# Performance work log

Hardware: AMD Instinct MI355X
Metric: run time of the kernel (lower is better)

The kernel has to match this reference:

```python
import jax, jax.numpy as jnp
import numpy as np

B, DIM, K, NH = 65536, 8, 64, 100
TOTAL = DIM * K


def setup_inputs() -> dict:
    key = jax.random.key(0)
    ks = jax.random.split(key, 14)
    e = jax.random.normal(ks[0], (B, DIM, K), dtype=jnp.float32)
    # strictly upper-triangular DAG adjacency: C[j, i] = 1 iff j < i (j is a parent of i)
    C = jnp.triu(jnp.ones((DIM, DIM), dtype=jnp.int32), k=1)
    sc = 0.05
    inp = {"e": e, "C": C}
    inp["sW1"] = jax.random.normal(ks[1], (TOTAL, NH), dtype=jnp.float32) * sc
    inp["sb1"] = jnp.zeros((NH,), dtype=jnp.float32)
    inp["sW2"] = jax.random.normal(ks[2], (NH, NH), dtype=jnp.float32) * sc
    inp["sb2"] = jnp.zeros((NH,), dtype=jnp.float32)
    inp["sW3"] = jax.random.normal(ks[3], (NH, K), dtype=jnp.float32) * sc
    inp["sb3"] = jnp.zeros((K,), dtype=jnp.float32)
    inp["tW1"] = jax.random.normal(ks[4], (TOTAL, NH), dtype=jnp.float32) * sc
    inp["tb1"] = jnp.zeros((NH,), dtype=jnp.float32)
    inp["tW2"] = jax.random.normal(ks[5], (NH, NH), dtype=jnp.float32) * sc
    inp["tb2"] = jnp.zeros((NH,), dtype=jnp.float32)
    inp["tW3"] = jax.random.normal(ks[6], (NH, K), dtype=jnp.float32) * sc
    inp["tb3"] = jnp.zeros((K,), dtype=jnp.float32)
    return inp


def _mlp(x, mask, W1, b1, W2, b2, W3, b3):
    # MLP.forward: net(x * mask); Linear->ReLU->Linear->ReLU->Linear->Sigmoid
    h = jax.nn.relu((x * mask) @ W1 + b1)
    h = jax.nn.relu(h @ W2 + b2)
    return jax.nn.sigmoid(h @ W3 + b3)


def reference(e, C, sW1, sb1, sW2, sb2, sW3, sb3, tW1, tb1, tW2, tb2, tW3, tb3):
    b, dim, k = e.shape
    total = dim * k
    # mask for step i: column C[:, i] with each entry repeated k times -> [total]
    # (if column i is all zeros, mask is zeros, matching the elif branch)
    masks = jnp.repeat(C.astype(e.dtype), k, axis=0).T  # [dim, total]
    e_steps = jnp.swapaxes(e, 0, 1)  # [dim, B, k]

    def step(z, xs):
        i, mask, e_i = xs
        zf = z.reshape(b, total)
        s = _mlp(zf, mask, sW1, sb1, sW2, sb2, sW3, sb3)  # [B, k]
        t = _mlp(zf, mask, tW1, tb1, tW2, tb2, tW3, tb3)  # [B, k]
        z = z.at[:, i, :].set(jnp.exp(s) * e_i + t)
        return z, jnp.sum(s, axis=1)

    z0 = jnp.zeros_like(e)
    z, ld_steps = jax.lax.scan(step, z0, (jnp.arange(dim), masks, e_steps))
    log_det = jnp.sum(ld_steps, axis=0)  # [B]
    return z, log_det
```

## Files before the change

### kernel.cpp

```cpp
#include <hip/hip_runtime.h>

#define B_SZ 65536
#define NH   100

typedef __bf16 bf16_t;
typedef __bf16 bf16x2 __attribute__((ext_vector_type(2)));
typedef __bf16 bf16x8 __attribute__((ext_vector_type(8)));
typedef float  f32x4  __attribute__((ext_vector_type(4)));

#define SZ_W2 14336
#define SZ_W3 8192
#define SZ_W1 7168
#define OFF_W3   28672
#define OFF_W1   45056
#define WS_TOTAL 145408

__global__ void prep_weights(const float* __restrict__ sW1, const float* __restrict__ sW2,
                             const float* __restrict__ sW3, const float* __restrict__ tW1,
                             const float* __restrict__ tW2, const float* __restrict__ tW3,
                             bf16_t* __restrict__ ws) {
  int idx = blockIdx.x * 256 + threadIdx.x;
  if (idx >= WS_TOTAL) return;
  float v = 0.f;
  if (idx < 2 * SZ_W2) {
    const float* W = (idx < SZ_W2) ? sW2 : tW2;
    int l = (idx < SZ_W2) ? idx : idx - SZ_W2;
    int j = l & 7, ln = (l >> 3) & 63, kc = (l >> 9) & 3, mt = l >> 11;
    int k = kc * 32 + (ln >> 4) * 8 + j;
    int m = mt * 16 + (ln & 15);
    v = (k < NH && m < NH) ? W[k * NH + m] : 0.f;
  } else if (idx < OFF_W1) {
    int l = idx - OFF_W3;
    const float* W = (l < SZ_W3) ? sW3 : tW3;
    l &= (SZ_W3 - 1);
    int j = l & 7, ln = (l >> 3) & 63, kc = (l >> 9) & 3, mt = l >> 11;
    int k = kc * 32 + (ln >> 4) * 8 + j;
    int m = mt * 16 + (ln & 15);
    v = (k < NH) ? W[k * 64 + m] : 0.f;
  } else {
    int l = idx - OFF_W1;
    int b = l / (2 * SZ_W1);
    int r2 = l - b * 2 * SZ_W1;
    const float* W = (r2 < SZ_W1) ? sW1 : tW1;
    int w = (r2 < SZ_W1) ? r2 : r2 - SZ_W1;
    int j = w & 7, ln = (w >> 3) & 63, kc = (w >> 9) & 1, mt = w >> 10;
    int k = kc * 32 + (ln >> 4) * 8 + j;
    int m = mt * 16 + (ln & 15);
    v = (m < NH) ? W[(b * 64 + k) * NH + m] : 0.f;
  }
  ws[idx] = (bf16_t)v;
}

__global__ void prep_bias(const float* __restrict__ sb1, const float* __restrict__ sb2,
                          const float* __restrict__ sb3, const float* __restrict__ tb1,
                          const float* __restrict__ tb2, const float* __restrict__ tb3,
                          float* __restrict__ fb) {
  int t = threadIdx.x;
  if (t < 112)       fb[t] = (t < NH) ? sb2[t] : 0.f;
  else if (t < 224)  fb[t] = (t - 112 < NH) ? tb2[t - 112] : 0.f;
  else if (t < 288)  fb[t] = sb3[t - 224];
  else if (t < 352)  fb[t] = tb3[t - 288];
  else if (t < 464)  fb[t] = (t - 352 < NH) ? sb1[t - 352] : 0.f;
  else if (t < 576)  fb[t] = (t - 464 < NH) ? tb1[t - 464] : 0.f;
}

__device__ __forceinline__ void gload_lds16(const void* gptr, void* lptr) {
  __builtin_amdgcn_global_load_lds(
      (const __attribute__((address_space(1))) unsigned int*)gptr,
      (__attribute__((address_space(3))) unsigned int*)lptr, 16, 0, 0);
}

__device__ __forceinline__ unsigned pk2(float a, float b) {
  bf16x2 t = {(bf16_t)a, (bf16_t)b};
  return __builtin_bit_cast(unsigned, t);
}

__device__ __forceinline__ bf16x8 build_bfrag(const unsigned* pkLo, const unsigned* pkHi,
                                              int idx0, int idx1, bool hiSel) {
  int l0 = __builtin_amdgcn_ds_bpermute(idx0, (int)pkLo[0]);
  int h0 = __builtin_amdgcn_ds_bpermute(idx0, (int)pkHi[0]);
  int l1 = __builtin_amdgcn_ds_bpermute(idx0, (int)pkLo[1]);
  int h1 = __builtin_amdgcn_ds_bpermute(idx0, (int)pkHi[1]);
  int l2 = __builtin_amdgcn_ds_bpermute(idx1, (int)pkLo[0]);
  int h2 = __builtin_amdgcn_ds_bpermute(idx1, (int)pkHi[0]);
  int l3 = __builtin_amdgcn_ds_bpermute(idx1, (int)pkLo[1]);
  int h3 = __builtin_amdgcn_ds_bpermute(idx1, (int)pkHi[1]);
  union { unsigned u[4]; bf16x8 v; } r;
  r.u[0] = (unsigned)(hiSel ? h0 : l0);
  r.u[1] = (unsigned)(hiSel ? h1 : l1);
  r.u[2] = (unsigned)(hiSel ? h2 : l2);
  r.u[3] = (unsigned)(hiSel ? h3 : l3);
  return r.v;
}

struct __align__(16) SMem {
  bf16_t w2[2 * SZ_W2];
  bf16_t w3[2 * SZ_W3];
  bf16_t w1[2][2 * SZ_W1];
  float  bias[512];
};

__global__ __launch_bounds__(512, 2) void flow_kernel(
    const float* __restrict__ e,
    const bf16_t* __restrict__ wf,
    const float* __restrict__ fb,
    float* __restrict__ out) {
  __shared__ SMem sm;

  const int tid  = threadIdx.x;
  const int wave = tid >> 6;
  const int lane = tid & 63;
  const int c    = lane & 15;
  const int Q    = lane >> 4;
  const int rowBase = blockIdx.x * 256 + wave * 32;

  const int  idx0  = 4 * (c + 32 * (Q & 1));
  const int  idx1  = idx0 + 64;
  const bool hiSel = (Q >= 2);

  {
    const char* g = (const char*)wf;
    char* l = (char*)&sm;
    const char* gb = (const char*)fb;
    #pragma unroll
    for (int t = 0; t < 15; ++t) {
      const int ch = t * 8 + wave;
      if (ch < 116)      gload_lds16(g + ch * 1024 + lane * 16, l + ch * 1024);
      else if (ch < 118) gload_lds16(gb + (ch - 116) * 1024 + lane * 16,
                                     (char*)sm.bias + (ch - 116) * 1024);
    }
  }

  f32x4 acc1S[2][7], acc1T[2][7];
  #pragma unroll
  for (int th = 0; th < 7; ++th) {
    const f32x4 vs = *(const f32x4*)(fb + 352 + th * 16 + Q * 4);
    const f32x4 vt = *(const f32x4*)(fb + 464 + th * 16 + Q * 4);
    acc1S[0][th] = vs; acc1S[1][th] = vs;
    acc1T[0][th] = vt; acc1T[1][th] = vt;
  }
  float ldacc[2] = {0.f, 0.f};

  __syncthreads();

  const float* lb2S = sm.bias;
  const float* lb2T = sm.bias + 112;
  const float* lb3S = sm.bias + 224;
  const float* lb3T = sm.bias + 288;

  auto run_net = [&](const f32x4 (&acc1)[2][7], const bf16_t* __restrict__ w2f,
                     const bf16_t* __restrict__ w3f, const float* __restrict__ lb2,
                     const float* __restrict__ lb3, f32x4 (&acc3)[2][4]) {
    unsigned pk[2][7][2];
    #pragma unroll
    for (int mt = 0; mt < 2; ++mt)
      #pragma unroll
      for (int th = 0; th < 7; ++th) {
        pk[mt][th][0] = pk2(fmaxf(acc1[mt][th][0], 0.f), fmaxf(acc1[mt][th][1], 0.f));
        pk[mt][th][1] = pk2(fmaxf(acc1[mt][th][2], 0.f), fmaxf(acc1[mt][th][3], 0.f));
      }
    f32x4 acc2[2][7];
    #pragma unroll
    for (int th = 0; th < 7; ++th) {
      const f32x4 bv = *(const f32x4*)(lb2 + th * 16 + Q * 4);
      acc2[0][th] = bv; acc2[1][th] = bv;
    }
    #pragma unroll
    for (int kc = 0; kc < 4; ++kc) {
      const int tlo = kc * 2, thi = (kc * 2 + 1 > 6) ? 6 : kc * 2 + 1;
      const bf16x8 b0 = build_bfrag(pk[0][tlo], pk[0][thi], idx0, idx1, hiSel);
      const bf16x8 b1 = build_bfrag(pk[1][tlo], pk[1][thi], idx0, idx1, hiSel);
      #pragma unroll
      for (int th = 0; th < 7; ++th) {
        const bf16x8 A = *(const bf16x8*)(w2f + ((th * 4 + kc) * 64 + lane) * 8);
        acc2[0][th] = __builtin_amdgcn_mfma_f32_16x16x32_bf16(A, b0, acc2[0][th], 0, 0, 0);
        acc2[1][th] = __builtin_amdgcn_mfma_f32_16x16x32_bf16(A, b1, acc2[1][th], 0, 0, 0);
      }
    }
    #pragma unroll
    for (int mt = 0; mt < 2; ++mt)
      #pragma unroll
      for (int th = 0; th < 7; ++th) {
        pk[mt][th][0] = pk2(fmaxf(acc2[mt][th][0], 0.f), fmaxf(acc2[mt][th][1], 0.f));
        pk[mt][th][1] = pk2(fmaxf(acc2[mt][th][2], 0.f), fmaxf(acc2[mt][th][3], 0.f));
      }
    #pragma unroll
    for (int ot = 0; ot < 4; ++ot) {
      const f32x4 bv = *(const f32x4*)(lb3 + ot * 16 + Q * 4);
      acc3[0][ot] = bv; acc3[1][ot] = bv;
    }
    #pragma unroll
    for (int kc = 0; kc < 4; ++kc) {
      const int tlo = kc * 2, thi = (kc * 2 + 1 > 6) ? 6 : kc * 2 + 1;
      const bf16x8 b0 = build_bfrag(pk[0][tlo], pk[0][thi], idx0, idx1, hiSel);
      const bf16x8 b1 = build_bfrag(pk[1][tlo], pk[1][thi], idx0, idx1, hiSel);
      #pragma unroll
      for (int ot = 0; ot < 4; ++ot) {
        const bf16x8 A = *(const bf16x8*)(w3f + ((ot * 4 + kc) * 64 + lane) * 8);
        acc3[0][ot] = __builtin_amdgcn_mfma_f32_16x16x32_bf16(A, b0, acc3[0][ot], 0, 0, 0);
        acc3[1][ot] = __builtin_amdgcn_mfma_f32_16x16x32_bf16(A, b1, acc3[1][ot], 0, 0, 0);
      }
    }
  };

  for (int i = 0; i < 8; ++i) {
    f32x4 acc3S[2][4], acc3T[2][4];
    run_net(acc1S, sm.w2,         sm.w3,         lb2S, lb3S, acc3S);
    run_net(acc1T, sm.w2 + SZ_W2, sm.w3 + SZ_W3, lb2T, lb3T, acc3T);

    unsigned zpk[2][4][2];
    #pragma unroll
    for (int mt = 0; mt < 2; ++mt) {
      #pragma unroll
      for (int ot = 0; ot < 4; ++ot) {
        const int off = (rowBase + mt * 16 + c) * 512 + i * 64 + ot * 16 + Q * 4;
        const f32x4 ev = *(const f32x4*)(e + off);
        f32x4 zv;
        float ss = 0.f;
        #pragma unroll
        for (int r = 0; r < 4; ++r) {
          const float sv = 1.f / (1.f + __expf(-acc3S[mt][ot][r]));
          const float tv = 1.f / (1.f + __expf(-acc3T[mt][ot][r]));
          zv[r] = __expf(sv) * ev[r] + tv;
          ss += sv;
        }
        __builtin_nontemporal_store(zv, (f32x4*)(out + off));
        zpk[mt][ot][0] = pk2(zv[0], zv[1]);
        zpk[mt][ot][1] = pk2(zv[2], zv[3]);
        ldacc[mt] += ss;
      }
    }

    if (i < 7) {
      __syncthreads();
      const bf16_t* __restrict__ w1b = sm.w1[i & 1];
      #pragma unroll
      for (int kc = 0; kc < 2; ++kc) {
        const bf16x8 b0 = build_bfrag(zpk[0][kc * 2], zpk[0][kc * 2 + 1], idx0, idx1, hiSel);
        const bf16x8 b1 = build_bfrag(zpk[1][kc * 2], zpk[1][kc * 2 + 1], idx0, idx1, hiSel);
        #pragma unroll
        for (int th = 0; th < 7; ++th) {
          const bf16x8 AS = *(const bf16x8*)(w1b + ((th * 2 + kc) * 64 + lane) * 8);
          const bf16x8 AT = *(const bf16x8*)(w1b + SZ_W1 + ((th * 2 + kc) * 64 + lane) * 8);
          acc1S[0][th] = __builtin_amdgcn_mfma_f32_16x16x32_bf16(AS, b0, acc1S[0][th], 0, 0, 0);
          acc1S[1][th] = __builtin_amdgcn_mfma_f32_16x16x32_bf16(AS, b1, acc1S[1][th], 0, 0, 0);
          acc1T[0][th] = __builtin_amdgcn_mfma_f32_16x16x32_bf16(AT, b0, acc1T[0][th], 0, 0, 0);
          acc1T[1][th] = __builtin_amdgcn_mfma_f32_16x16x32_bf16(AT, b1, acc1T[1][th], 0, 0, 0);
        }
      }
      if (i < 6) {
        const char* g = (const char*)wf + 90112 + (i + 1) * 28672;
        char* l = (char*)sm.w1[(i + 1) & 1];
        #pragma unroll
        for (int t = 0; t < 4; ++t) {
          const int ch = t * 8 + wave;
          if (ch < 28) gload_lds16(g + ch * 1024 + lane * 16, l + ch * 1024);
        }
      }
    }
  }

  #pragma unroll
  for (int mt = 0; mt < 2; ++mt) {
    float v = ldacc[mt];
    v += __shfl_xor(v, 16);
    v += __shfl_xor(v, 32);
    if (Q == 0) out[B_SZ * 512 + rowBase + mt * 16 + c] = v;
  }
}

extern "C" void kernel_launch(void* const* d_in, const int* in_sizes, int n_in,
                              void* d_out, int out_size, void* d_ws, size_t ws_size,
                              hipStream_t stream) {
  (void)in_sizes; (void)n_in; (void)out_size; (void)ws_size;
  const float* e   = (const float*)d_in[0];
  const float* sW1 = (const float*)d_in[2];
  const float* sb1 = (const float*)d_in[3];
  const float* sW2 = (const float*)d_in[4];
  const float* sb2 = (const float*)d_in[5];
  const float* sW3 = (const float*)d_in[6];
  const float* sb3 = (const float*)d_in[7];
  const float* tW1 = (const float*)d_in[8];
  const float* tb1 = (const float*)d_in[9];
  const float* tW2 = (const float*)d_in[10];
  const float* tb2 = (const float*)d_in[11];
  const float* tW3 = (const float*)d_in[12];
  const float* tb3 = (const float*)d_in[13];
  bf16_t* ws = (bf16_t*)d_ws;
  float*  fb = (float*)(ws + WS_TOTAL);
  float* out = (float*)d_out;

  prep_weights<<<(WS_TOTAL + 255) / 256, 256, 0, stream>>>(sW1, sW2, sW3, tW1, tW2, tW3, ws);
  prep_bias<<<1, 576, 0, stream>>>(sb1, sb2, sb3, tb1, tb2, tb3, fb);
  flow_kernel<<<256, 512, 0, stream>>>(e, ws, fb, out);
}
```

Baseline: 335.3 us.

## Use permlane swaps for B-fragments and stream W1 from global

The ds_bpermute-based fragment builder is replaced with v_permlane32/16_swap register swaps. The double-buffered LDS copy of W1 and its per-step __syncthreads are dropped, and W1 fragments are read straight from global memory (L2-cached). This shrinks LDS usage and removes block-wide barriers. The sigmoid division also becomes a hardware reciprocal. The trade-off is global-load latency inside the layer-1 MFMA loop and slightly lower reciprocal precision.

```diff
diff --git a/kernel.cpp b/kernel.cpp
--- a/kernel.cpp
+++ b/kernel.cpp
@@ -75,28 +75,23 @@
   return __builtin_bit_cast(unsigned, t);
 }
 
-__device__ __forceinline__ bf16x8 build_bfrag(const unsigned* pkLo, const unsigned* pkHi,
-                                              int idx0, int idx1, bool hiSel) {
-  int l0 = __builtin_amdgcn_ds_bpermute(idx0, (int)pkLo[0]);
-  int h0 = __builtin_amdgcn_ds_bpermute(idx0, (int)pkHi[0]);
-  int l1 = __builtin_amdgcn_ds_bpermute(idx0, (int)pkLo[1]);
-  int h1 = __builtin_amdgcn_ds_bpermute(idx0, (int)pkHi[1]);
-  int l2 = __builtin_amdgcn_ds_bpermute(idx1, (int)pkLo[0]);
-  int h2 = __builtin_amdgcn_ds_bpermute(idx1, (int)pkHi[0]);
-  int l3 = __builtin_amdgcn_ds_bpermute(idx1, (int)pkLo[1]);
-  int h3 = __builtin_amdgcn_ds_bpermute(idx1, (int)pkHi[1]);
+__device__ __forceinline__ void plswap(unsigned &x, unsigned &y) {
+  asm("v_permlane32_swap_b32 %0, %1" : "+v"(x), "+v"(y));
+  asm("v_permlane16_swap_b32 %0, %1" : "+v"(x), "+v"(y));
+}
+
+__device__ __forceinline__ bf16x8 build_bfrag(unsigned lo0, unsigned lo1,
+                                              unsigned hi0, unsigned hi1) {
+  plswap(lo0, hi0);
+  plswap(lo1, hi1);
   union { unsigned u[4]; bf16x8 v; } r;
-  r.u[0] = (unsigned)(hiSel ? h0 : l0);
-  r.u[1] = (unsigned)(hiSel ? h1 : l1);
-  r.u[2] = (unsigned)(hiSel ? h2 : l2);
-  r.u[3] = (unsigned)(hiSel ? h3 : l3);
+  r.u[0] = lo0; r.u[1] = lo1; r.u[2] = hi0; r.u[3] = hi1;
   return r.v;
 }
 
 struct __align__(16) SMem {
   bf16_t w2[2 * SZ_W2];
   bf16_t w3[2 * SZ_W3];
-  bf16_t w1[2][2 * SZ_W1];
   float  bias[512];
 };
 
@@ -114,20 +109,16 @@
   const int Q    = lane >> 4;
   const int rowBase = blockIdx.x * 256 + wave * 32;
 
-  const int  idx0  = 4 * (c + 32 * (Q & 1));
-  const int  idx1  = idx0 + 64;
-  const bool hiSel = (Q >= 2);
-
   {
     const char* g = (const char*)wf;
     char* l = (char*)&sm;
     const char* gb = (const char*)fb;
     #pragma unroll
-    for (int t = 0; t < 15; ++t) {
+    for (int t = 0; t < 12; ++t) {
       const int ch = t * 8 + wave;
-      if (ch < 116)      gload_lds16(g + ch * 1024 + lane * 16, l + ch * 1024);
-      else if (ch < 118) gload_lds16(gb + (ch - 116) * 1024 + lane * 16,
-                                     (char*)sm.bias + (ch - 116) * 1024);
+      if (ch < 88)      gload_lds16(g + ch * 1024 + lane * 16, l + ch * 1024);
+      else if (ch < 90) gload_lds16(gb + (ch - 88) * 1024 + lane * 16,
+                                    (char*)sm.bias + (ch - 88) * 1024);
     }
   }
 
@@ -168,8 +159,8 @@
     #pragma unroll
     for (int kc = 0; kc < 4; ++kc) {
       const int tlo = kc * 2, thi = (kc * 2 + 1 > 6) ? 6 : kc * 2 + 1;
-      const bf16x8 b0 = build_bfrag(pk[0][tlo], pk[0][thi], idx0, idx1, hiSel);
-      const bf16x8 b1 = build_bfrag(pk[1][tlo], pk[1][thi], idx0, idx1, hiSel);
+      const bf16x8 b0 = build_bfrag(pk[0][tlo][0], pk[0][tlo][1], pk[0][thi][0], pk[0][thi][1]);
+      const bf16x8 b1 = build_bfrag(pk[1][tlo][0], pk[1][tlo][1], pk[1][thi][0], pk[1][thi][1]);
       #pragma unroll
       for (int th = 0; th < 7; ++th) {
         const bf16x8 A = *(const bf16x8*)(w2f + ((th * 4 + kc) * 64 + lane) * 8);
@@ -192,8 +183,8 @@
     #pragma unroll
     for (int kc = 0; kc < 4; ++kc) {
       const int tlo = kc * 2, thi = (kc * 2 + 1 > 6) ? 6 : kc * 2 + 1;
-      const bf16x8 b0 = build_bfrag(pk[0][tlo], pk[0][thi], idx0, idx1, hiSel);
-      const bf16x8 b1 = build_bfrag(pk[1][tlo], pk[1][thi], idx0, idx1, hiSel);
+      const bf16x8 b0 = build_bfrag(pk[0][tlo][0], pk[0][tlo][1], pk[0][thi][0], pk[0][thi][1]);
+      const bf16x8 b1 = build_bfrag(pk[1][tlo][0], pk[1][tlo][1], pk[1][thi][0], pk[1][thi][1]);
       #pragma unroll
       for (int ot = 0; ot < 4; ++ot) {
         const bf16x8 A = *(const bf16x8*)(w3f + ((ot * 4 + kc) * 64 + lane) * 8);
@@ -219,8 +210,8 @@
         float ss = 0.f;
         #pragma unroll
         for (int r = 0; r < 4; ++r) {
-          const float sv = 1.f / (1.f + __expf(-acc3S[mt][ot][r]));
-          const float tv = 1.f / (1.f + __expf(-acc3T[mt][ot][r]));
+          const float sv = __builtin_amdgcn_rcpf(1.f + __expf(-acc3S[mt][ot][r]));
+          const float tv = __builtin_amdgcn_rcpf(1.f + __expf(-acc3T[mt][ot][r]));
           zv[r] = __expf(sv) * ev[r] + tv;
           ss += sv;
         }
@@ -232,29 +223,21 @@
     }
 
     if (i < 7) {
-      __syncthreads();
-      const bf16_t* __restrict__ w1b = sm.w1[i & 1];
+      const bf16_t* __restrict__ w1g = wf + OFF_W1 + i * 2 * SZ_W1;
       #pragma unroll
       for (int kc = 0; kc < 2; ++kc) {
-        const bf16x8 b0 = build_bfrag(zpk[0][kc * 2], zpk[0][kc * 2 + 1], idx0, idx1, hiSel);
-        const bf16x8 b1 = build_bfrag(zpk[1][kc * 2], zpk[1][kc * 2 + 1], idx0, idx1, hiSel);
+        const bf16x8 b0 = build_bfrag(zpk[0][kc * 2][0], zpk[0][kc * 2][1],
+                                      zpk[0][kc * 2 + 1][0], zpk[0][kc * 2 + 1][1]);
+        const bf16x8 b1 = build_bfrag(zpk[1][kc * 2][0], zpk[1][kc * 2][1],
+                                      zpk[1][kc * 2 + 1][0], zpk[1][kc * 2 + 1][1]);
         #pragma unroll
         for (int th = 0; th < 7; ++th) {
-          const bf16x8 AS = *(const bf16x8*)(w1b + ((th * 2 + kc) * 64 + lane) * 8);
-          const bf16x8 AT = *(const bf16x8*)(w1b + SZ_W1 + ((th * 2 + kc) * 64 + lane) * 8);
+          const bf16x8 AS = *(const bf16x8*)(w1g + ((th * 2 + kc) * 64 + lane) * 8);
+          const bf16x8 AT = *(const bf16x8*)(w1g + SZ_W1 + ((th * 2 + kc) * 64 + lane) * 8);
           acc1S[0][th] = __builtin_amdgcn_mfma_f32_16x16x32_bf16(AS, b0, acc1S[0][th], 0, 0, 0);
           acc1S[1][th] = __builtin_amdgcn_mfma_f32_16x16x32_bf16(AS, b1, acc1S[1][th], 0, 0, 0);
           acc1T[0][th] = __builtin_amdgcn_mfma_f32_16x16x32_bf16(AT, b0, acc1T[0][th], 0, 0, 0);
           acc1T[1][th] = __builtin_amdgcn_mfma_f32_16x16x32_bf16(AT, b1, acc1T[1][th], 0, 0, 0);
-        }
-      }
-      if (i < 6) {
-        const char* g = (const char*)wf + 90112 + (i + 1) * 28672;
-        char* l = (char*)sm.w1[(i + 1) & 1];
-        #pragma unroll
-        for (int t = 0; t < 4; ++t) {
-          const int ch = t * 8 + wave;
-          if (ch < 28) gload_lds16(g + ch * 1024 + lane * 16, l + ch * 1024);
         }
       }
     }
```

Result: slower. 393.2 us (+17.3%).
